# Kernel optimization log

Measured on AMD Instinct MI355X. Metric: run time of the kernel, lower is better.

## Reference

```python
import jax, jax.numpy as jnp
import numpy as np

VOCAB, EMB, FEAT = 30000, 300, 2048
B, NQ, NW, NK = 256, 32, 12, 64


def setup_inputs() -> dict:
    key = jax.random.key(0)
    ks = jax.random.split(key, 10)
    return {
        "wv": jax.random.normal(ks[0], (VOCAB, EMB), jnp.float32),
        "Wf": jax.random.normal(ks[1], (EMB, FEAT), jnp.float32) * 0.02,
        "bf": jax.random.normal(ks[2], (EMB,), jnp.float32) * 0.02,
        "Wp": jax.random.normal(ks[3], (EMB, EMB), jnp.float32) * 0.05,
        "bp": jax.random.normal(ks[4], (EMB,), jnp.float32) * 0.02,
        "Wm": jax.random.normal(ks[5], (EMB, EMB), jnp.float32) * 0.05,
        "bm": jax.random.normal(ks[6], (EMB,), jnp.float32) * 0.02,
        "feature": jax.random.normal(ks[7], (B, NK, FEAT), jnp.float32),
        "query": jax.random.randint(ks[8], (B, NQ, NW), 0, VOCAB),
        "label": jax.random.randint(ks[9], (B, NK), 0, VOCAB),
    }


def reference(wv, Wf, bf, Wp, bp, Wm, bm, feature, query, label):
    # Dropouts act as identity in eval mode.
    eps = 1e-5
    q_emb = wv[query]                                   # [B, queries, words, D]
    k_emb = wv[label] + feature @ Wf.T + bf             # [B, objects, D]
    scale = 1.0 / np.sqrt(EMB)
    att = jnp.einsum('byqd,bkd->byqk', q_emb, k_emb) * scale
    att = jax.nn.softmax(att, axis=-1)                  # over objects
    q_max_att = jnp.max(att, axis=3)                    # [B, queries, words]
    neg_inf = -jnp.finfo(q_max_att.dtype).max
    q_max_att = jnp.where(query == 0, neg_inf, q_max_att)
    q_max_norm_att = jax.nn.softmax(q_max_att, axis=-1) / 5.0
    p_emb = jnp.einsum('byq,byqd->byd', q_max_norm_att, q_emb)  # [B, queries, D]
    p_emb = (p_emb @ Wp.T + bp) + eps * (p_emb @ Wm.T + bm)
    return p_emb, k_emb
```

## Files before the change

kernel.cpp:

```cpp
#include <hip/hip_runtime.h>

typedef unsigned short u16;
typedef unsigned int u32;
typedef __bf16 bf16x8 __attribute__((ext_vector_type(8)));
typedef float f32x4 __attribute__((ext_vector_type(4)));

#if defined(__has_builtin)
#  if __has_builtin(__builtin_amdgcn_cvt_pk_bf16_f32)
#    define PK_BF16 1
#  endif
#endif

__device__ __forceinline__ u16 f2bu(float f){
  u32 u = __float_as_uint(f);
  return (u16)((u + 0x7fffu + ((u >> 16) & 1u)) >> 16);
}
__device__ __forceinline__ float b2f(u16 u){
  union { float f; u32 i; } v; v.i = ((u32)u) << 16; return v.f;
}
__device__ __forceinline__ u32 pkbf(float a, float b){
#ifdef PK_BF16
  typedef __bf16 bf16x2 __attribute__((ext_vector_type(2)));
  union { bf16x2 h; u32 u; } c;
  c.h = __builtin_amdgcn_cvt_pk_bf16_f32(a, b);
  return c.u;
#else
  return (u32)f2bu(a) | ((u32)f2bu(b) << 16);
#endif
}

__global__ __launch_bounds__(256) void prep_wc(
    const float* __restrict__ Wp, const float* __restrict__ bp,
    const float* __restrict__ Wm, const float* __restrict__ bm,
    u16* __restrict__ Wc, float* __restrict__ bc)
{
  int idx = blockIdx.x * 256 + threadIdx.x;
  if (idx < 384 * 160) {
    int n = idx / 160, k = (idx % 160) * 2;
    float v0 = 0.f, v1 = 0.f;
    if (n < 300 && k < 300) {
      v0 = Wp[n * 300 + k]     + 1e-5f * Wm[n * 300 + k];
      v1 = Wp[n * 300 + k + 1] + 1e-5f * Wm[n * 300 + k + 1];
    }
    ((u32*)Wc)[idx] = pkbf(v0, v1);
    if (idx < 384) bc[idx] = (idx < 300) ? bp[idx] + 1e-5f * bm[idx] : 0.f;
  }
}

__global__ __launch_bounds__(256) void prep_wv16(
    const float* __restrict__ wv, u16* __restrict__ wv16)
{
  int idx = blockIdx.x * 256 + threadIdx.x;
  if (idx < 30000 * 160) {
    int row = idx / 160, k = (idx % 160) * 2;
    float v0 = 0.f, v1 = 0.f;
    if (k < 300) {
      v0 = wv[(size_t)row * 300 + k];
      v1 = wv[(size_t)row * 300 + k + 1];
    }
    ((u32*)wv16)[idx] = pkbf(v0, v1);
  }
}

__global__ __launch_bounds__(256) void gemm0_kernel(
    const float* __restrict__ A, const float* __restrict__ B,
    const float* __restrict__ bias,
    const int* __restrict__ label, const float* __restrict__ wv,
    float* __restrict__ C, u16* __restrict__ kemb16)
{
  __shared__ __align__(16) u16 As[128 * 32];
  __shared__ __align__(16) u16 Bs[128 * 32];
  const int lda = 2048, ldb = 2048, K = 2048, nbn = 3, nsrc = 300;
  int t = threadIdx.x;
  int bm = (blockIdx.x / nbn) * 128;
  int bn = (blockIdx.x % nbn) * 128;
  int lane = t & 63, w = t >> 6;
  int wm = (w >> 1) * 64, wn = (w & 1) * 64;

  f32x4 acc[4][4];
  for (int i = 0; i < 4; i++)
    for (int j = 0; j < 4; j++)
      for (int r = 0; r < 4; r++) acc[i][j][r] = 0.f;

  int mrow = lane & 15, q = lane >> 4;

  for (int kk = 0; kk < K; kk += 32) {
    #pragma unroll
    for (int p = 0; p < 2; p++) {
      int idx = t + p * 256;
      int row = idx >> 2, ch = idx & 3;
      int brow = bn + row;
      if (brow >= nsrc) brow = 0;
      const float4* ap = (const float4*)&A[(size_t)(bm + row) * lda + kk + ch * 8];
      float4 a0 = ap[0], a1 = ap[1];
      const float4* bpp = (const float4*)&B[(size_t)brow * ldb + kk + ch * 8];
      float4 b0 = bpp[0], b1 = bpp[1];
      union { u32 u[4]; uint4 v; } pa, pb;
      pa.u[0] = pkbf(a0.x, a0.y); pa.u[1] = pkbf(a0.z, a0.w);
      pa.u[2] = pkbf(a1.x, a1.y); pa.u[3] = pkbf(a1.z, a1.w);
      pb.u[0] = pkbf(b0.x, b0.y); pb.u[1] = pkbf(b0.z, b0.w);
      pb.u[2] = pkbf(b1.x, b1.y); pb.u[3] = pkbf(b1.z, b1.w);
      *(uint4*)&As[idx * 8] = pa.v;
      *(uint4*)&Bs[idx * 8] = pb.v;
    }
    __syncthreads();

    bf16x8 af[4], bfr[4];
    #pragma unroll
    for (int i = 0; i < 4; i++)
      af[i] = *(const bf16x8*)&As[(wm + i * 16 + mrow) * 32 + q * 8];
    #pragma unroll
    for (int j = 0; j < 4; j++)
      bfr[j] = *(const bf16x8*)&Bs[(wn + j * 16 + mrow) * 32 + q * 8];
    #pragma unroll
    for (int i = 0; i < 4; i++)
      #pragma unroll
      for (int j = 0; j < 4; j++)
        acc[i][j] = __builtin_amdgcn_mfma_f32_16x16x32_bf16(
            af[i], bfr[j], acc[i][j], 0, 0, 0);
    __syncthreads();
  }

  #pragma unroll
  for (int i = 0; i < 4; i++)
    #pragma unroll
    for (int j = 0; j < 4; j++) {
      int col = bn + wn + j * 16 + (lane & 15);
      int rb = bm + wm + i * 16 + (lane >> 4) * 4;
      #pragma unroll
      for (int r = 0; r < 4; r++) {
        int m = rb + r;
        if (col < 300) {
          float v = acc[i][j][r];
          v += bias[col] + wv[(size_t)label[m] * 300 + col];
          C[(size_t)m * 300 + col] = v;
          if (kemb16) kemb16[(size_t)m * 320 + col] = f2bu(v);
        } else if (kemb16 && col < 320) {
          kemb16[(size_t)m * 320 + col] = 0;
        }
      }
    }
}

template <int FULL>
__global__ __launch_bounds__(256) void attn_kernel(
    const float* __restrict__ wv, const u16* __restrict__ wv16,
    const int* __restrict__ query,
    const float* __restrict__ kout, const u16* __restrict__ kemb16,
    u16* __restrict__ praw)
{
  __shared__ __align__(16) u16 ke[64 * 328];
  __shared__ __align__(16) int qoff[192];
  __shared__ __align__(16) float awd[192];
  __shared__ __align__(16) float wt[192];

  int blk = blockIdx.x, b = blk >> 1, bh = blk & 1;
  int t = threadIdx.x;
  int lane = t & 63, w = t >> 6;

  if (FULL) {
    for (int i = t; i < 2560; i += 256) {
      int row = i / 40, ch = i % 40;
      *(uint4*)&ke[row * 328 + ch * 8] =
          *(const uint4*)&kemb16[(size_t)(b * 64 + row) * 320 + ch * 8];
    }
  } else {
    for (int i = t; i < 4800; i += 256) {
      int row = i / 75, c4 = i % 75;
      float4 v = *(const float4*)&kout[(size_t)(b * 64 + row) * 300 + c4 * 4];
      *(u32*)&ke[row * 328 + c4 * 4]     = pkbf(v.x, v.y);
      *(u32*)&ke[row * 328 + c4 * 4 + 2] = pkbf(v.z, v.w);
    }
    for (int i = t; i < 640; i += 256) {
      int row = i / 10, c2 = i % 10;
      *(u32*)&ke[row * 328 + 300 + c2 * 2] = 0;
    }
  }
  if (t < 192)
    qoff[t] = query[b * 384 + bh * 192 + t] * (FULL ? 320 : 300);
  __syncthreads();

  int mrow = lane & 15, q = lane >> 4;
  f32x4 acc[3][4];
  #pragma unroll
  for (int i = 0; i < 3; i++)
    #pragma unroll
    for (int j = 0; j < 4; j++)
      #pragma unroll
      for (int r = 0; r < 4; r++) acc[i][j][r] = 0.f;

  int base[3];
  #pragma unroll
  for (int i = 0; i < 3; i++) base[i] = qoff[w * 48 + i * 16 + mrow];
  int keb = mrow * 328 + q * 8;

  for (int k0 = 0; k0 < 320; k0 += 32) {
    bf16x8 af[3], bfr[4];
    #pragma unroll
    for (int i = 0; i < 3; i++) {
      if (FULL) {
        af[i] = *(const bf16x8*)&wv16[(size_t)base[i] + k0 + q * 8];
      } else {
        int cs = k0 + q * 8;
        union { u32 u[4]; bf16x8 h; } c;
        if (cs + 8 <= 300) {
          const float4* p = (const float4*)&wv[(size_t)base[i] + cs];
          float4 x = p[0], y = p[1];
          c.u[0] = pkbf(x.x, x.y); c.u[1] = pkbf(x.z, x.w);
          c.u[2] = pkbf(y.x, y.y); c.u[3] = pkbf(y.z, y.w);
        } else if (cs < 300) {
          float4 x = *(const float4*)&wv[(size_t)base[i] + 296];
          c.u[0] = pkbf(x.x, x.y); c.u[1] = pkbf(x.z, x.w);
          c.u[2] = 0; c.u[3] = 0;
        } else {
          c.u[0] = 0; c.u[1] = 0; c.u[2] = 0; c.u[3] = 0;
        }
        af[i] = c.h;
      }
    }
    #pragma unroll
    for (int j = 0; j < 4; j++)
      bfr[j] = *(const bf16x8*)&ke[j * 16 * 328 + keb + k0];
    #pragma unroll
    for (int i = 0; i < 3; i++)
      #pragma unroll
      for (int j = 0; j < 4; j++)
        acc[i][j] = __builtin_amdgcn_mfma_f32_16x16x32_bf16(
            af[i], bfr[j], acc[i][j], 0, 0, 0);
  }

  const float scale = 0.05773502691896258f;
  #pragma unroll
  for (int i = 0; i < 3; i++)
    #pragma unroll
    for (int r = 0; r < 4; r++) {
      float mx = fmaxf(fmaxf(acc[i][0][r], acc[i][1][r]),
                       fmaxf(acc[i][2][r], acc[i][3][r]));
      #pragma unroll
      for (int d = 1; d < 16; d <<= 1)
        mx = fmaxf(mx, __shfl_xor(mx, d));
      float se = 0.f;
      #pragma unroll
      for (int j = 0; j < 4; j++)
        se += __expf((acc[i][j][r] - mx) * scale);
      #pragma unroll
      for (int d = 1; d < 16; d <<= 1)
        se += __shfl_xor(se, d);
      if (mrow == 0) {
        int wl = w * 48 + i * 16 + q * 4 + r;
        awd[wl] = (qoff[wl] == 0) ? -3.402823466e38f : (1.0f / se);
      }
    }
  __syncthreads();

  if (t < 16) {
    int yb = t * 12;
    float m2 = -3.402823466e38f;
    for (int i = 0; i < 12; i++) m2 = fmaxf(m2, awd[yb + i]);
    float e[12], s2 = 0.f;
    for (int i = 0; i < 12; i++) { e[i] = __expf(awd[yb + i] - m2); s2 += e[i]; }
    float inv = 0.2f / s2;
    for (int i = 0; i < 12; i++) wt[yb + i] = e[i] * inv;
  }
  __syncthreads();

  #pragma unroll
  for (int yy = 0; yy < 4; yy++) {
    int yl = w * 4 + yy;
    int row = b * 32 + bh * 16 + yl;
    #pragma unroll
    for (int c = 0; c < 5; c++) {
      int d = c * 64 + lane;
      float s = 0.f;
      if (d < 300) {
        for (int i = 0; i < 12; i++) {
          float g = wt[yl * 12 + i];
          int off = qoff[yl * 12 + i];
          s += g * (FULL ? b2f(wv16[(size_t)off + d]) : wv[(size_t)off + d]);
        }
      }
      praw[(size_t)row * 320 + d] = f2bu(s);
    }
  }
}

__global__ __launch_bounds__(256) void proj_kernel(
    const u16* __restrict__ praw, const u16* __restrict__ Wc,
    const float* __restrict__ bc, float* __restrict__ P)
{
  __shared__ __align__(16) u16 As[128 * 32];
  __shared__ __align__(16) u16 Bs[128 * 32];
  int t = threadIdx.x;
  int bm = (blockIdx.x / 3) * 128;
  int bn = (blockIdx.x % 3) * 128;
  int lane = t & 63, w = t >> 6;
  int wm = (w >> 1) * 64, wn = (w & 1) * 64;

  f32x4 acc[4][4];
  for (int i = 0; i < 4; i++)
    for (int j = 0; j < 4; j++)
      for (int r = 0; r < 4; r++) acc[i][j][r] = 0.f;

  int mrow = lane & 15, q = lane >> 4;

  for (int kk = 0; kk < 320; kk += 32) {
    #pragma unroll
    for (int p = 0; p < 2; p++) {
      int idx = t + p * 256;
      int row = idx >> 2, ch = idx & 3;
      *(uint4*)&As[idx * 8] =
          *(const uint4*)&praw[(size_t)(bm + row) * 320 + kk + ch * 8];
      *(uint4*)&Bs[idx * 8] =
          *(const uint4*)&Wc[(size_t)(bn + row) * 320 + kk + ch * 8];
    }
    __syncthreads();

    bf16x8 af[4], bfr[4];
    #pragma unroll
    for (int i = 0; i < 4; i++)
      af[i] = *(const bf16x8*)&As[(wm + i * 16 + mrow) * 32 + q * 8];
    #pragma unroll
    for (int j = 0; j < 4; j++)
      bfr[j] = *(const bf16x8*)&Bs[(wn + j * 16 + mrow) * 32 + q * 8];
    #pragma unroll
    for (int i = 0; i < 4; i++)
      #pragma unroll
      for (int j = 0; j < 4; j++)
        acc[i][j] = __builtin_amdgcn_mfma_f32_16x16x32_bf16(
            af[i], bfr[j], acc[i][j], 0, 0, 0);
    __syncthreads();
  }

  #pragma unroll
  for (int i = 0; i < 4; i++)
    #pragma unroll
    for (int j = 0; j < 4; j++) {
      int col = bn + wn + j * 16 + (lane & 15);
      if (col >= 300) continue;
      int rb = bm + wm + i * 16 + (lane >> 4) * 4;
      #pragma unroll
      for (int r = 0; r < 4; r++)
        P[(size_t)(rb + r) * 300 + col] = acc[i][j][r] + bc[col];
    }
}

extern "C" void kernel_launch(void* const* d_in, const int* in_sizes, int n_in,
                              void* d_out, int out_size, void* d_ws,
                              size_t ws_size, hipStream_t stream)
{
  const float* wv      = (const float*)d_in[0];
  const float* Wf      = (const float*)d_in[1];
  const float* bf      = (const float*)d_in[2];
  const float* Wp      = (const float*)d_in[3];
  const float* bp      = (const float*)d_in[4];
  const float* Wm      = (const float*)d_in[5];
  const float* bm      = (const float*)d_in[6];
  const float* feature = (const float*)d_in[7];
  const int*   query   = (const int*)d_in[8];
  const int*   label   = (const int*)d_in[9];

  float* out   = (float*)d_out;
  float* p_out = out;
  float* k_out = out + 2457600;

  char* ws = (char*)d_ws;
  int full = ws_size >= (size_t)35175936;
  u16 *wv16 = 0, *kemb16 = 0, *praw, *Wc;
  float* bc;
  if (full) {
    wv16   = (u16*)ws;
    kemb16 = (u16*)(ws + 19200000);
    praw   = (u16*)(ws + 29685760);
    Wc     = (u16*)(ws + 34928640);
    bc     = (float*)(ws + 35174400);
  } else {
    praw   = (u16*)ws;
    Wc     = (u16*)(ws + 5242880);
    bc     = (float*)(ws + 5488640);
  }

  prep_wc<<<240, 256, 0, stream>>>(Wp, bp, Wm, bm, Wc, bc);
  if (full)
    prep_wv16<<<18750, 256, 0, stream>>>(wv, wv16);

  gemm0_kernel<<<384, 256, 0, stream>>>(feature, Wf, bf, label, wv,
                                        k_out, kemb16);

  if (full)
    attn_kernel<1><<<512, 256, 0, stream>>>(wv, wv16, query, k_out,
                                            kemb16, praw);
  else
    attn_kernel<0><<<512, 256, 0, stream>>>(wv, wv16, query, k_out,
                                            kemb16, praw);

  proj_kernel<<<192, 256, 0, stream>>>(praw, Wc, bc, p_out);
}
```

Before: 376.7 us.

## Pre-convert GEMM operands to bf16 and stage tiles via global_load_lds

Adds prep kernels that convert feature and Wf to bf16 in workspace, so gemm0 can load tiles straight into LDS with global_load_lds instead of loading fp32 and converting in registers. proj_kernel also switches to global_load_lds. attn_kernel pads its key LDS stride, prefetches the next query-embedding fragment one step ahead, and vectorises the weighted-sum stage to 8 bf16 elements per lane. The conversion pass adds an extra full read and write of the 64MB feature tensor, and the new path only runs when the workspace is large enough.

```diff
diff --git a/kernel.cpp b/kernel.cpp
--- a/kernel.cpp
+++ b/kernel.cpp
@@ -28,6 +28,11 @@
   return (u32)f2bu(a) | ((u32)f2bu(b) << 16);
 #endif
 }
+__device__ __forceinline__ void glds16(const u16* g, u16* l){
+  __builtin_amdgcn_global_load_lds(
+      (const __attribute__((address_space(1))) void*)g,
+      (__attribute__((address_space(3))) void*)l, 16, 0, 0);
+}
 
 __global__ __launch_bounds__(256) void prep_wc(
     const float* __restrict__ Wp, const float* __restrict__ bp,
@@ -62,15 +67,43 @@
   }
 }
 
+__global__ __launch_bounds__(256) void prep_f16(
+    const float* __restrict__ src, u16* __restrict__ dst, int n4)
+{
+  int i = blockIdx.x * 256 + threadIdx.x;
+  if (i < n4) {
+    float4 v = ((const float4*)src)[i];
+    uint2 o; o.x = pkbf(v.x, v.y); o.y = pkbf(v.z, v.w);
+    ((uint2*)dst)[i] = o;
+  }
+}
+
+__global__ __launch_bounds__(256) void prep_wf16(
+    const float* __restrict__ Wf, u16* __restrict__ Wf16)
+{
+  int i = blockIdx.x * 256 + threadIdx.x;
+  if (i < 384 * 1024) {
+    int row = i >> 10, c2 = (i & 1023) * 2;
+    float v0 = 0.f, v1 = 0.f;
+    if (row < 300) {
+      v0 = Wf[(size_t)row * 2048 + c2];
+      v1 = Wf[(size_t)row * 2048 + c2 + 1];
+    }
+    ((u32*)Wf16)[i] = pkbf(v0, v1);
+  }
+}
+
+template <int GLDS>
 __global__ __launch_bounds__(256) void gemm0_kernel(
     const float* __restrict__ A, const float* __restrict__ B,
+    const u16* __restrict__ Af16, const u16* __restrict__ Bf16,
     const float* __restrict__ bias,
     const int* __restrict__ label, const float* __restrict__ wv,
     float* __restrict__ C, u16* __restrict__ kemb16)
 {
   __shared__ __align__(16) u16 As[128 * 32];
   __shared__ __align__(16) u16 Bs[128 * 32];
-  const int lda = 2048, ldb = 2048, K = 2048, nbn = 3, nsrc = 300;
+  const int lda = 2048, K = 2048, nbn = 3, nsrc = 300;
   int t = threadIdx.x;
   int bm = (blockIdx.x / nbn) * 128;
   int bn = (blockIdx.x % nbn) * 128;
@@ -85,23 +118,36 @@
   int mrow = lane & 15, q = lane >> 4;
 
   for (int kk = 0; kk < K; kk += 32) {
-    #pragma unroll
-    for (int p = 0; p < 2; p++) {
-      int idx = t + p * 256;
-      int row = idx >> 2, ch = idx & 3;
-      int brow = bn + row;
-      if (brow >= nsrc) brow = 0;
-      const float4* ap = (const float4*)&A[(size_t)(bm + row) * lda + kk + ch * 8];
-      float4 a0 = ap[0], a1 = ap[1];
-      const float4* bpp = (const float4*)&B[(size_t)brow * ldb + kk + ch * 8];
-      float4 b0 = bpp[0], b1 = bpp[1];
-      union { u32 u[4]; uint4 v; } pa, pb;
-      pa.u[0] = pkbf(a0.x, a0.y); pa.u[1] = pkbf(a0.z, a0.w);
-      pa.u[2] = pkbf(a1.x, a1.y); pa.u[3] = pkbf(a1.z, a1.w);
-      pb.u[0] = pkbf(b0.x, b0.y); pb.u[1] = pkbf(b0.z, b0.w);
-      pb.u[2] = pkbf(b1.x, b1.y); pb.u[3] = pkbf(b1.z, b1.w);
-      *(uint4*)&As[idx * 8] = pa.v;
-      *(uint4*)&Bs[idx * 8] = pb.v;
+    if (GLDS) {
+      int r0 = w * 32;
+      int rl = lane >> 2, ch = lane & 3;
+      #pragma unroll
+      for (int p = 0; p < 2; p++) {
+        int row = r0 + p * 16 + rl;
+        glds16(&Af16[(size_t)(bm + row) * 2048 + kk + ch * 8],
+               &As[(r0 + p * 16) * 32]);
+        glds16(&Bf16[(size_t)(bn + row) * 2048 + kk + ch * 8],
+               &Bs[(r0 + p * 16) * 32]);
+      }
+    } else {
+      #pragma unroll
+      for (int p = 0; p < 2; p++) {
+        int idx = t + p * 256;
+        int row = idx >> 2, ch = idx & 3;
+        int brow = bn + row;
+        if (brow >= nsrc) brow = 0;
+        const float4* ap = (const float4*)&A[(size_t)(bm + row) * lda + kk + ch * 8];
+        float4 a0 = ap[0], a1 = ap[1];
+        const float4* bpp = (const float4*)&B[(size_t)brow * lda + kk + ch * 8];
+        float4 b0 = bpp[0], b1 = bpp[1];
+        union { u32 u[4]; uint4 v; } pa, pb;
+        pa.u[0] = pkbf(a0.x, a0.y); pa.u[1] = pkbf(a0.z, a0.w);
+        pa.u[2] = pkbf(a1.x, a1.y); pa.u[3] = pkbf(a1.z, a1.w);
+        pb.u[0] = pkbf(b0.x, b0.y); pb.u[1] = pkbf(b0.z, b0.w);
+        pb.u[2] = pkbf(b1.x, b1.y); pb.u[3] = pkbf(b1.z, b1.w);
+        *(uint4*)&As[idx * 8] = pa.v;
+        *(uint4*)&Bs[idx * 8] = pb.v;
+      }
     }
     __syncthreads();
 
@@ -142,6 +188,7 @@
     }
 }
 
+#define KES 344
 template <int FULL>
 __global__ __launch_bounds__(256) void attn_kernel(
     const float* __restrict__ wv, const u16* __restrict__ wv16,
@@ -149,7 +196,7 @@
     const float* __restrict__ kout, const u16* __restrict__ kemb16,
     u16* __restrict__ praw)
 {
-  __shared__ __align__(16) u16 ke[64 * 328];
+  __shared__ __align__(16) u16 ke[64 * KES];
   __shared__ __align__(16) int qoff[192];
   __shared__ __align__(16) float awd[192];
   __shared__ __align__(16) float wt[192];
@@ -161,19 +208,19 @@
   if (FULL) {
     for (int i = t; i < 2560; i += 256) {
       int row = i / 40, ch = i % 40;
-      *(uint4*)&ke[row * 328 + ch * 8] =
+      *(uint4*)&ke[row * KES + ch * 8] =
           *(const uint4*)&kemb16[(size_t)(b * 64 + row) * 320 + ch * 8];
     }
   } else {
     for (int i = t; i < 4800; i += 256) {
       int row = i / 75, c4 = i % 75;
       float4 v = *(const float4*)&kout[(size_t)(b * 64 + row) * 300 + c4 * 4];
-      *(u32*)&ke[row * 328 + c4 * 4]     = pkbf(v.x, v.y);
-      *(u32*)&ke[row * 328 + c4 * 4 + 2] = pkbf(v.z, v.w);
+      *(u32*)&ke[row * KES + c4 * 4]     = pkbf(v.x, v.y);
+      *(u32*)&ke[row * KES + c4 * 4 + 2] = pkbf(v.z, v.w);
     }
     for (int i = t; i < 640; i += 256) {
       int row = i / 10, c2 = i % 10;
-      *(u32*)&ke[row * 328 + 300 + c2 * 2] = 0;
+      *(u32*)&ke[row * KES + 300 + c2 * 2] = 0;
     }
   }
   if (t < 192)
@@ -192,14 +239,23 @@
   int base[3];
   #pragma unroll
   for (int i = 0; i < 3; i++) base[i] = qoff[w * 48 + i * 16 + mrow];
-  int keb = mrow * 328 + q * 8;
+  int keb = mrow * KES + q * 8;
+
+  bf16x8 afn[3];
+  #pragma unroll
+  for (int i = 0; i < 3; i++) {
+    if (FULL)
+      afn[i] = *(const bf16x8*)&wv16[(size_t)base[i] + q * 8];
+  }
 
   for (int k0 = 0; k0 < 320; k0 += 32) {
     bf16x8 af[3], bfr[4];
     #pragma unroll
     for (int i = 0; i < 3; i++) {
       if (FULL) {
-        af[i] = *(const bf16x8*)&wv16[(size_t)base[i] + k0 + q * 8];
+        af[i] = afn[i];
+        if (k0 + 32 < 320)
+          afn[i] = *(const bf16x8*)&wv16[(size_t)base[i] + k0 + 32 + q * 8];
       } else {
         int cs = k0 + q * 8;
         union { u32 u[4]; bf16x8 h; } c;
@@ -220,7 +276,7 @@
     }
     #pragma unroll
     for (int j = 0; j < 4; j++)
-      bfr[j] = *(const bf16x8*)&ke[j * 16 * 328 + keb + k0];
+      bfr[j] = *(const bf16x8*)&ke[j * 16 * KES + keb + k0];
     #pragma unroll
     for (int i = 0; i < 3; i++)
       #pragma unroll
@@ -268,18 +324,33 @@
   for (int yy = 0; yy < 4; yy++) {
     int yl = w * 4 + yy;
     int row = b * 32 + bh * 16 + yl;
-    #pragma unroll
-    for (int c = 0; c < 5; c++) {
-      int d = c * 64 + lane;
-      float s = 0.f;
-      if (d < 300) {
+    if (FULL) {
+      if (lane < 40) {
+        float s[8];
+        #pragma unroll
+        for (int e = 0; e < 8; e++) s[e] = 0.f;
         for (int i = 0; i < 12; i++) {
           float g = wt[yl * 12 + i];
-          int off = qoff[yl * 12 + i];
-          s += g * (FULL ? b2f(wv16[(size_t)off + d]) : wv[(size_t)off + d]);
+          union { uint4 v; u16 h[8]; } qv;
+          qv.v = *(const uint4*)&wv16[(size_t)qoff[yl * 12 + i] + lane * 8];
+          #pragma unroll
+          for (int e = 0; e < 8; e++) s[e] += g * b2f(qv.h[e]);
         }
-      }
-      praw[(size_t)row * 320 + d] = f2bu(s);
+        union { uint4 v; u16 h[8]; } o;
+        #pragma unroll
+        for (int e = 0; e < 8; e++) o.h[e] = f2bu(s[e]);
+        *(uint4*)&praw[(size_t)row * 320 + lane * 8] = o.v;
+      }
+    } else {
+      #pragma unroll
+      for (int c = 0; c < 5; c++) {
+        int d = c * 64 + lane;
+        float s = 0.f;
+        if (d < 300)
+          for (int i = 0; i < 12; i++)
+            s += wt[yl * 12 + i] * wv[(size_t)qoff[yl * 12 + i] + d];
+        praw[(size_t)row * 320 + d] = f2bu(s);
+      }
     }
   }
 }
@@ -304,14 +375,15 @@
   int mrow = lane & 15, q = lane >> 4;
 
   for (int kk = 0; kk < 320; kk += 32) {
+    int r0 = w * 32;
+    int rl = lane >> 2, ch = lane & 3;
     #pragma unroll
     for (int p = 0; p < 2; p++) {
-      int idx = t + p * 256;
-      int row = idx >> 2, ch = idx & 3;
-      *(uint4*)&As[idx * 8] =
-          *(const uint4*)&praw[(size_t)(bm + row) * 320 + kk + ch * 8];
-      *(uint4*)&Bs[idx * 8] =
-          *(const uint4*)&Wc[(size_t)(bn + row) * 320 + kk + ch * 8];
+      int row = r0 + p * 16 + rl;
+      glds16(&praw[(size_t)(bm + row) * 320 + kk + ch * 8],
+             &As[(r0 + p * 16) * 32]);
+      glds16(&Wc[(size_t)(bn + row) * 320 + kk + ch * 8],
+             &Bs[(r0 + p * 16) * 32]);
     }
     __syncthreads();
 
@@ -364,10 +436,19 @@
   float* k_out = out + 2457600;
 
   char* ws = (char*)d_ws;
-  int full = ws_size >= (size_t)35175936;
-  u16 *wv16 = 0, *kemb16 = 0, *praw, *Wc;
+  int t2 = ws_size >= (size_t)103857664;
+  int t1 = ws_size >= (size_t)35175936;
+  u16 *f16 = 0, *wf16 = 0, *wv16 = 0, *kemb16 = 0, *praw, *Wc;
   float* bc;
-  if (full) {
+  if (t2) {
+    f16    = (u16*)ws;
+    wv16   = (u16*)(ws + 67108864);
+    kemb16 = (u16*)(ws + 86308864);
+    praw   = (u16*)(ws + 96794624);
+    Wc     = (u16*)(ws + 102037504);
+    wf16   = (u16*)(ws + 102283264);
+    bc     = (float*)(ws + 103856128);
+  } else if (t1) {
     wv16   = (u16*)ws;
     kemb16 = (u16*)(ws + 19200000);
     praw   = (u16*)(ws + 29685760);
@@ -380,13 +461,19 @@
   }
 
   prep_wc<<<240, 256, 0, stream>>>(Wp, bp, Wm, bm, Wc, bc);
-  if (full)
+  if (t1 || t2)
     prep_wv16<<<18750, 256, 0, stream>>>(wv, wv16);
-
-  gemm0_kernel<<<384, 256, 0, stream>>>(feature, Wf, bf, label, wv,
-                                        k_out, kemb16);
-
-  if (full)
+  if (t2) {
+    prep_f16<<<32768, 256, 0, stream>>>(feature, f16, 8388608);
+    prep_wf16<<<1536, 256, 0, stream>>>(Wf, wf16);
+    gemm0_kernel<1><<<384, 256, 0, stream>>>(feature, Wf, f16, wf16, bf,
+                                             label, wv, k_out, kemb16);
+  } else {
+    gemm0_kernel<0><<<384, 256, 0, stream>>>(feature, Wf, 0, 0, bf,
+                                             label, wv, k_out, kemb16);
+  }
+
+  if (t1 || t2)
     attn_kernel<1><<<512, 256, 0, stream>>>(wv, wv16, query, k_out,
                                             kemb16, praw);
   else
```

New measurement: 374.3 us. About the same (-0.6%).
